# Kernel optimization log

Measured on AMD Instinct MI355X. Metric: run time of the kernel, lower is better.

The kernel has to match this reference:

```python
import jax, jax.numpy as jnp
import numpy as np

DIM = 2048
ORDER = 1
# upper-triangular index pairs (i<j), row-major over i then j — matches torch loop order
_IU_ROWS, _IU_COLS = np.triu_indices(DIM, k=1)


def setup_inputs() -> dict:
    key = jax.random.key(0)
    k1, k2 = jax.random.split(key)
    num_params = DIM * (DIM - 1) // 2
    x = jax.random.normal(k1, (4, 4096, DIM), dtype=jnp.float32)
    angles = jax.random.normal(k2, (num_params,), dtype=jnp.float32) * 0.01
    bias = jnp.zeros((DIM,), dtype=jnp.float32)
    return {"x": x, "angles": angles, "bias": bias}


def _skew_symmetric(angles):
    # A[i,j] = angles[k], A[j,i] = -angles[k] for upper-tri (i<j)
    A = jnp.zeros((DIM, DIM), dtype=angles.dtype)
    A = A.at[_IU_ROWS, _IU_COLS].set(angles)
    return A - A.T


def _cayley_approx(A, order=ORDER):
    # W = (I + A + ... + A^order) @ (I + A)
    I = jnp.eye(DIM, dtype=A.dtype)
    inv_approx = I
    A_power = A
    for _ in range(order):
        inv_approx = inv_approx + A_power
        A_power = A_power @ A
    return inv_approx @ (I + A)


def reference(x, angles, bias):
    A = _skew_symmetric(angles)
    W = _cayley_approx(A)
    # [b, s, d] @ [d, d] -> [b, s, d]
    out = jnp.einsum('bsd,de->bse', x, W) + bias
    return out
```

## Files before the change

kernel.cpp:

```cpp
#include <hip/hip_runtime.h>
#include <stdint.h>

#define DIM 2048

typedef short short8 __attribute__((ext_vector_type(8)));
typedef float f32x4 __attribute__((ext_vector_type(4)));

__device__ __forceinline__ unsigned short f2bf(float f) {
    union { float f; unsigned int u; } v;
    v.f = f;
    unsigned int r = v.u + 0x7FFFu + ((v.u >> 16) & 1u);
    return (unsigned short)(r >> 16);
}
__device__ __forceinline__ float bf2f(unsigned short u) {
    union { unsigned int u; float f; } v;
    v.u = ((unsigned int)u) << 16;
    return v.f;
}

__device__ __forceinline__ void async16(const unsigned short* g, unsigned short* l) {
    __builtin_amdgcn_global_load_lds(
        (__attribute__((address_space(1))) void*)(uintptr_t)g,
        (__attribute__((address_space(3))) void*)(uintptr_t)l,
        16, 0, 0);
}

__global__ __launch_bounds__(256) void build_A_tiled(const float* __restrict__ ang,
                                                     unsigned short* __restrict__ A) {
    __shared__ float tile[64][65];
    int b = blockIdx.x;
    int ti = 0, rem = b;
    while (rem >= 32 - ti) { rem -= 32 - ti; ++ti; }
    const int tj = ti + rem;
    const int t  = threadIdx.x;
    const int lj = t & 63;
    const int lw = t >> 6;
    const bool diag = (ti == tj);

#pragma unroll
    for (int m = 0; m < 16; ++m) {
        const int li = lw * 16 + m;
        const int i = ti * 64 + li;
        const int j = tj * 64 + lj;
        float v = 0.0f;
        if (i < j) v = ang[i * (4095 - i) / 2 + (j - i - 1)];
        tile[li][lj] = v;
    }
    __syncthreads();

#pragma unroll
    for (int m = 0; m < 16; ++m) {
        const int li = lw * 16 + m;
        float v;
        if (diag) {
            if (li < lj)      v =  tile[li][lj];
            else if (li > lj) v = -tile[lj][li];
            else              v = 0.0f;
        } else {
            v = tile[li][lj];
        }
        A[(size_t)(ti * 64 + li) * DIM + tj * 64 + lj] = f2bf(v);
    }
    if (!diag) {
#pragma unroll
        for (int m = 0; m < 16; ++m) {
            const int li = lw * 16 + m;
            A[(size_t)(tj * 64 + li) * DIM + ti * 64 + lj] = f2bf(-tile[lj][li]);
        }
    }
}

__global__ __launch_bounds__(256) void s64sym_cvt(
        const unsigned short* __restrict__ A,
        unsigned short* __restrict__ Wt,
        const float* __restrict__ x,
        unsigned short* __restrict__ xbf) {
    __shared__ __align__(16) unsigned short smem[12288];
    unsigned short* ldsA = smem;
    unsigned short* ldsB = smem + 4096;
    float* ldsT = (float*)smem;

    if (blockIdx.x >= 528) {
        const int i = ((blockIdx.x - 528) * 256 + threadIdx.x) * 4;
        const float4 v = *(const float4*)(x + i);
        ushort4 o;
        o.x = f2bf(v.x); o.y = f2bf(v.y); o.z = f2bf(v.z); o.w = f2bf(v.w);
        *(ushort4*)(xbf + i) = o;
        return;
    }

    const int K = DIM, N = DIM;
    const int t = threadIdx.x;
    const int swz = (blockIdx.x & 7) * 66 + (blockIdx.x >> 3);
    int ti = 0, rem = swz;
    while (rem >= 32 - ti) { rem -= 32 - ti; ++ti; }
    const int tj = ti + rem;
    const int bm = ti * 64;
    const int bn = tj * 64;

    const int lane = t & 63;
    const int wave = t >> 6;
    const int waveM = (wave >> 1) * 32;
    const int waveN = (wave & 1) * 32;
    const int fm = lane & 15;
    const int fq = lane >> 4;

    f32x4 acc[2][2];
#pragma unroll
    for (int i = 0; i < 2; ++i)
#pragma unroll
        for (int j = 0; j < 2; ++j)
            acc[i][j] = (f32x4){0.f, 0.f, 0.f, 0.f};

    const int trow   = t >> 3;
    const int tchunk = (t & 7) ^ (trow & 7);
    const unsigned short* gA = A + (size_t)(bm + trow) * K + tchunk * 8;
    const unsigned short* gB = A + (size_t)(bn + trow) * K + tchunk * 8;
    const size_t rowskip = (size_t)32 * K;
    unsigned short* lA = ldsA + t * 8;
    unsigned short* lB = ldsB + t * 8;

    for (int kt = 0; kt < K; kt += 64) {
        __syncthreads();
        async16(gA + kt, lA);
        async16(gA + kt + rowskip, lA + 2048);
        async16(gB + kt, lB);
        async16(gB + kt + rowskip, lB + 2048);
        __syncthreads();

#pragma unroll
        for (int ks = 0; ks < 2; ++ks) {
            short8 af[2], bfv[2];
#pragma unroll
            for (int i = 0; i < 2; ++i) {
                const int rowA = waveM + i * 16 + fm;
                const int rowB = waveN + i * 16 + fm;
                af[i]  = *(const short8*)(ldsA + rowA * 64 + (((ks << 2) + fq) ^ (rowA & 7)) * 8);
                bfv[i] = *(const short8*)(ldsB + rowB * 64 + (((ks << 2) + fq) ^ (rowB & 7)) * 8);
            }
#pragma unroll
            for (int i = 0; i < 2; ++i)
#pragma unroll
                for (int j = 0; j < 2; ++j)
                    acc[i][j] = __builtin_amdgcn_mfma_f32_16x16x32_bf16(
                        af[i], bfv[j], acc[i][j], 0, 0, 0);
        }
    }

    __syncthreads();
#pragma unroll
    for (int i = 0; i < 2; ++i) {
#pragma unroll
        for (int j = 0; j < 2; ++j) {
            const int lj = waveN + j * 16 + fm;
            const int gj = bn + lj;
#pragma unroll
            for (int r = 0; r < 4; ++r) {
                const int li = waveM + i * 16 + fq * 4 + r;
                const int gi = bm + li;
                const float a = bf2f(A[(size_t)gi * N + gj]);
                const float s = acc[i][j][r];
                const float d = (gi == gj) ? 1.0f : 0.0f;
                Wt[(size_t)gi * N + gj] = f2bf(d - 2.0f * a - s);
                ldsT[lj * 65 + li] = d + 2.0f * a - s;
            }
        }
    }
    __syncthreads();
    {
        const int r  = t >> 2;
        const int cb = (t & 3) * 16;
        unsigned short o[16];
#pragma unroll
        for (int u = 0; u < 16; ++u)
            o[u] = f2bf(ldsT[r * 65 + cb + u]);
        *(short8*)(Wt + (size_t)(bn + r) * N + bm + cb)     = *(short8*)(o);
        *(short8*)(Wt + (size_t)(bn + r) * N + bm + cb + 8) = *(short8*)(o + 8);
    }
}


#define WAITV(N) asm volatile("s_waitcnt vmcnt(" #N ")" ::: "memory")
#define BAR() do { asm volatile("" ::: "memory"); __builtin_amdgcn_s_barrier(); asm volatile("" ::: "memory"); } while (0)

#define STG_A(BUF, R0, KT) async16(gA + (size_t)(R0) * 2048 + (KT), &ldsA[BUF][(R0) * 64 + t * 8])
#define STG_B(BUF, R0, KT) async16(gB + (size_t)(R0) * 2048 + (KT), &ldsB[BUF][(R0) * 64 + t * 8])

#define READ_A_(BUF, IH) do { \
    _Pragma("unroll") \
    for (int ii = 0; ii < 4; ++ii) { \
        const int row  = waveM + (IH) * 64 + ii * 16 + fm; \
        const int base = row * 64; \
        af[ii][0] = *(const short8*)(&ldsA[BUF][base + ((fq    ) ^ (row & 7)) * 8]); \
        af[ii][1] = *(const short8*)(&ldsA[BUF][base + ((fq + 4) ^ (row & 7)) * 8]); \
    } } while (0)

#define READ_B_(BUF, JH) do { \
    _Pragma("unroll") \
    for (int jj = 0; jj < 2; ++jj) { \
        const int row  = (JH) * 128 + wn * 32 + jj * 16 + fm; \
        const int base = row * 64; \
        bfr[JH][jj][0] = *(const short8*)(&ldsB[BUF][base + ((fq    ) ^ (row & 7)) * 8]); \
        bfr[JH][jj][1] = *(const short8*)(&ldsB[BUF][base + ((fq + 4) ^ (row & 7)) * 8]); \
    } } while (0)

#define MMAQ(IH, JH) do { \
    __builtin_amdgcn_s_setprio(1); \
    _Pragma("unroll") \
    for (int ks = 0; ks < 2; ++ks) \
    _Pragma("unroll") \
    for (int ii = 0; ii < 4; ++ii) \
    _Pragma("unroll") \
    for (int jj = 0; jj < 2; ++jj) \
        acc[(IH) * 4 + ii][(JH) * 2 + jj] = __builtin_amdgcn_mfma_f32_16x16x32_bf16( \
            af[ii][ks], bfr[JH][jj][ks], acc[(IH) * 4 + ii][(JH) * 2 + jj], 0, 0, 0); \
    __builtin_amdgcn_s_setprio(0); \
} while (0)

#define TILE(BUF, KTN, PRE, VN, NXT) do { \
     \
    BAR(); \
    if (PRE) { STG_A(BUF, 0, KTN); STG_A(BUF, 128, KTN); STG_B(BUF, 0, KTN); STG_B(BUF, 64, KTN); } \
    MMAQ(0, 0); \
    READ_B_(BUF, 1); \
     \
    BAR(); \
    if (PRE) { STG_B(BUF, 128, KTN); STG_B(BUF, 192, KTN); } \
    MMAQ(0, 1); \
    READ_A_(BUF, 1); \
     \
    WAITV(VN); \
    BAR(); \
    if (PRE) { STG_A(BUF, 64, KTN); STG_A(BUF, 192, KTN); } \
    MMAQ(1, 0); \
    if (NXT) READ_B_((BUF) ^ 1, 0); \
     \
    BAR(); \
    MMAQ(1, 1); \
    if (NXT) READ_A_((BUF) ^ 1, 0); \
} while (0)

#define TILE_LAST(BUF) do { \
    BAR(); MMAQ(0, 0); READ_B_(BUF, 1); \
    BAR(); MMAQ(0, 1); READ_A_(BUF, 1); \
    BAR(); MMAQ(1, 0); \
    MMAQ(1, 1); \
} while (0)

__global__ __launch_bounds__(512, 2) void gemm_main(
        const unsigned short* __restrict__ Aop,
        const unsigned short* __restrict__ Bop,
        int M, int N, int K,
        const float* __restrict__ bias,
        float* __restrict__ out) {
    __shared__ __align__(16) unsigned short ldsA[2][256 * 64];
    __shared__ __align__(16) unsigned short ldsB[2][256 * 64];

    const int t    = threadIdx.x;
    const int flat = blockIdx.y * 8 + blockIdx.x;
    const int swz  = (flat & 7) * 64 + (flat >> 3);
    const int bn   = (swz & 7) * 256;
    const int bm   = (swz >> 3) * 256;
    const int lane = t & 63;
    const int wave = t >> 6;
    const int wm   = wave >> 2;
    const int wn   = wave & 3;
    const int waveM = wm * 128;
    const int fm = lane & 15;
    const int fq = lane >> 4;

    f32x4 acc[8][4];
#pragma unroll
    for (int i = 0; i < 8; ++i)
#pragma unroll
        for (int j = 0; j < 4; ++j)
            acc[i][j] = (f32x4){0.f, 0.f, 0.f, 0.f};

    short8 af[4][2];
    short8 bfr[2][2][2];

    const int trow   = t >> 3;
    const int tchunk = (t & 7) ^ (trow & 7);
    const unsigned short* gA = Aop + (size_t)(bm + trow) * 2048 + tchunk * 8;
    const unsigned short* gB = Bop + (size_t)(bn + trow) * 2048 + tchunk * 8;

    STG_A(0, 0, 0);   STG_A(0, 128, 0);  STG_B(0, 0, 0);   STG_B(0, 64, 0);
    STG_B(0, 128, 0); STG_B(0, 192, 0);  STG_A(0, 64, 0);  STG_A(0, 192, 0);
    STG_A(1, 0, 64);  STG_A(1, 128, 64); STG_B(1, 0, 64);  STG_B(1, 64, 64);
    STG_B(1, 128, 64);STG_B(1, 192, 64); STG_A(1, 64, 64); STG_A(1, 192, 64);
    WAITV(8);
    BAR();
    READ_A_(0, 0);
    READ_B_(0, 0);

#pragma unroll 1
    for (int it = 0; it < 15; ++it) {
        const int kt = it * 128;
        TILE(0, kt + 128, 1, 6, 1);
        TILE(1, kt + 192, 1, 6, 1);
    }
    TILE(0, 0, 0, 0, 1);
    TILE_LAST(1);

#pragma unroll
    for (int i = 0; i < 8; ++i) {
        const int row0 = bm + waveM + i * 16 + fq * 4;
#pragma unroll
        for (int j = 0; j < 4; ++j) {
            const int col = bn + (j >> 1) * 128 + wn * 32 + (j & 1) * 16 + fm;
            const float b = bias[col];
#pragma unroll
            for (int r = 0; r < 4; ++r)
                out[(size_t)(row0 + r) * 2048 + col] = acc[i][j][r] + b;
        }
    }
}

extern "C" void kernel_launch(void* const* d_in, const int* in_sizes, int n_in,
                              void* d_out, int out_size, void* d_ws, size_t ws_size,
                              hipStream_t stream) {
    const float* x      = (const float*)d_in[0];
    const float* angles = (const float*)d_in[1];
    const float* bias   = (const float*)d_in[2];
    float* out = (float*)d_out;

    char* ws = (char*)d_ws;
    unsigned short* Abf = (unsigned short*)ws;
    unsigned short* Wt  = (unsigned short*)(ws + (8u << 20));
    unsigned short* xbf = (unsigned short*)(ws + (16u << 20));

    const int M = 4 * 4096;

    build_A_tiled<<<528, 256, 0, stream>>>(angles, Abf);

    s64sym_cvt<<<528 + 32768, 256, 0, stream>>>(Abf, Wt, x, xbf);

    gemm_main<<<dim3(DIM / 256, M / 256), 512, 0, stream>>>(
        xbf, Wt, M, DIM, DIM, bias, out);
}
```

Baseline: 349.6 us.

## Load B fragments directly from global into registers, bypassing LDS

```diff
diff --git a/kernel.cpp b/kernel.cpp
--- a/kernel.cpp
+++ b/kernel.cpp
@@ -184,7 +184,6 @@
 #define BAR() do { asm volatile("" ::: "memory"); __builtin_amdgcn_s_barrier(); asm volatile("" ::: "memory"); } while (0)
 
 #define STG_A(BUF, R0, KT) async16(gA + (size_t)(R0) * 2048 + (KT), &ldsA[BUF][(R0) * 64 + t * 8])
-#define STG_B(BUF, R0, KT) async16(gB + (size_t)(R0) * 2048 + (KT), &ldsB[BUF][(R0) * 64 + t * 8])
 
 #define READ_A_(BUF, IH) do { \
     _Pragma("unroll") \
@@ -195,14 +194,13 @@
         af[ii][1] = *(const short8*)(&ldsA[BUF][base + ((fq + 4) ^ (row & 7)) * 8]); \
     } } while (0)
 
-#define READ_B_(BUF, JH) do { \
-    _Pragma("unroll") \
-    for (int jj = 0; jj < 2; ++jj) { \
-        const int row  = (JH) * 128 + wn * 32 + jj * 16 + fm; \
-        const int base = row * 64; \
-        bfr[JH][jj][0] = *(const short8*)(&ldsB[BUF][base + ((fq    ) ^ (row & 7)) * 8]); \
-        bfr[JH][jj][1] = *(const short8*)(&ldsB[BUF][base + ((fq + 4) ^ (row & 7)) * 8]); \
-    } } while (0)
+#define LOAD_B(JH, KT) do { \
+    _Pragma("unroll") \
+    for (int jj = 0; jj < 2; ++jj) \
+    _Pragma("unroll") \
+    for (int ks = 0; ks < 2; ++ks) \
+        bfr[JH][jj][ks] = *(const short8*)(gBf + (size_t)((JH) * 128 + jj * 16) * 2048 + (KT) + ks * 32); \
+} while (0)
 
 #define MMAQ(IH, JH) do { \
     __builtin_amdgcn_s_setprio(1); \
@@ -217,34 +215,33 @@
     __builtin_amdgcn_s_setprio(0); \
 } while (0)
 
-#define TILE(BUF, KTN, PRE, VN, NXT) do { \
+#define TILE(BUF, KTC, PRE, NXT) do { \
      \
     BAR(); \
-    if (PRE) { STG_A(BUF, 0, KTN); STG_A(BUF, 128, KTN); STG_B(BUF, 0, KTN); STG_B(BUF, 64, KTN); } \
+    if (PRE) { STG_A(BUF, 0, (KTC) + 128); STG_A(BUF, 128, (KTC) + 128); } \
+    LOAD_B(1, KTC); \
     MMAQ(0, 0); \
-    READ_B_(BUF, 1); \
      \
+    WAITV(12); \
     BAR(); \
-    if (PRE) { STG_B(BUF, 128, KTN); STG_B(BUF, 192, KTN); } \
     MMAQ(0, 1); \
     READ_A_(BUF, 1); \
      \
-    WAITV(VN); \
     BAR(); \
-    if (PRE) { STG_A(BUF, 64, KTN); STG_A(BUF, 192, KTN); } \
+    if (PRE) { STG_A(BUF, 64, (KTC) + 128); STG_A(BUF, 192, (KTC) + 128); } \
     MMAQ(1, 0); \
-    if (NXT) READ_B_((BUF) ^ 1, 0); \
+    if (NXT) LOAD_B(0, (KTC) + 64); \
      \
     BAR(); \
     MMAQ(1, 1); \
     if (NXT) READ_A_((BUF) ^ 1, 0); \
 } while (0)
 
-#define TILE_LAST(BUF) do { \
-    BAR(); MMAQ(0, 0); READ_B_(BUF, 1); \
-    BAR(); MMAQ(0, 1); READ_A_(BUF, 1); \
+#define TILE_LAST(BUF, KTC) do { \
+    BAR(); LOAD_B(1, KTC); MMAQ(0, 0); \
+    WAITV(12); BAR(); MMAQ(0, 1); READ_A_(BUF, 1); \
     BAR(); MMAQ(1, 0); \
-    MMAQ(1, 1); \
+    BAR(); MMAQ(1, 1); \
 } while (0)
 
 __global__ __launch_bounds__(512, 2) void gemm_main(
@@ -254,7 +251,6 @@
         const float* __restrict__ bias,
         float* __restrict__ out) {
     __shared__ __align__(16) unsigned short ldsA[2][256 * 64];
-    __shared__ __align__(16) unsigned short ldsB[2][256 * 64];
 
     const int t    = threadIdx.x;
     const int flat = blockIdx.y * 8 + blockIdx.x;
@@ -281,26 +277,26 @@
 
     const int trow   = t >> 3;
     const int tchunk = (t & 7) ^ (trow & 7);
-    const unsigned short* gA = Aop + (size_t)(bm + trow) * 2048 + tchunk * 8;
-    const unsigned short* gB = Bop + (size_t)(bn + trow) * 2048 + tchunk * 8;
-
-    STG_A(0, 0, 0);   STG_A(0, 128, 0);  STG_B(0, 0, 0);   STG_B(0, 64, 0);
-    STG_B(0, 128, 0); STG_B(0, 192, 0);  STG_A(0, 64, 0);  STG_A(0, 192, 0);
-    STG_A(1, 0, 64);  STG_A(1, 128, 64); STG_B(1, 0, 64);  STG_B(1, 64, 64);
-    STG_B(1, 128, 64);STG_B(1, 192, 64); STG_A(1, 64, 64); STG_A(1, 192, 64);
-    WAITV(8);
+    const unsigned short* gA  = Aop + (size_t)(bm + trow) * 2048 + tchunk * 8;
+    const unsigned short* gBf = Bop + (size_t)(bn + wn * 32 + fm) * 2048 + fq * 8;
+
+    STG_A(0, 0, 0);   STG_A(0, 128, 0);
+    STG_A(0, 64, 0);  STG_A(0, 192, 0);
+    STG_A(1, 0, 64);  STG_A(1, 128, 64);
+    STG_A(1, 64, 64); STG_A(1, 192, 64);
+    LOAD_B(0, 0);
+    WAITV(10);
     BAR();
     READ_A_(0, 0);
-    READ_B_(0, 0);
 
 #pragma unroll 1
     for (int it = 0; it < 15; ++it) {
         const int kt = it * 128;
-        TILE(0, kt + 128, 1, 6, 1);
-        TILE(1, kt + 192, 1, 6, 1);
-    }
-    TILE(0, 0, 0, 0, 1);
-    TILE_LAST(1);
+        TILE(0, kt,      1, 1);
+        TILE(1, kt + 64, 1, 1);
+    }
+    TILE(0, 1920, 0, 1);
+    TILE_LAST(1, 1984);
 
 #pragma unroll
     for (int i = 0; i < 8; ++i) {
```

Measured after the change: 435.4 us. 24.5% more time.
